# Optimization experiments

Measured on AMD Instinct MI355X. Metric: run time of the kernel, lower is better.

## Reference

```python
import jax, jax.numpy as jnp
import numpy as np

N_NODES = 50000
NEG_SLOPE = 0.2


def _gat_conv(x, edge_index, W, att_src, att_dst, bias, heads, out_ch, concat):
    """PyG-style GATConv (add_self_loops=True, negative_slope=0.2).
    x: [N, F_in], edge_index: [2, E] (row=src, row=dst), W: [F_in, heads*out_ch],
    att_src/att_dst: [heads, out_ch], bias: [heads*out_ch] or [out_ch]."""
    N = x.shape[0]
    # add self-loops
    loops = jnp.arange(N, dtype=edge_index.dtype)
    src = jnp.concatenate([edge_index[0], loops])
    dst = jnp.concatenate([edge_index[1], loops])

    h = (x @ W).reshape(N, heads, out_ch)                 # [N, H, C]
    a_src = jnp.einsum('nhc,hc->nh', h, att_src)          # [N, H]
    a_dst = jnp.einsum('nhc,hc->nh', h, att_dst)          # [N, H]

    e = a_src[src] + a_dst[dst]                           # [E', H]
    e = jnp.where(e >= 0, e, NEG_SLOPE * e)               # leaky_relu

    # segment softmax over incoming edges of each dst node
    e_max = jax.ops.segment_max(e, dst, num_segments=N)   # [N, H]
    e_max = jnp.where(jnp.isfinite(e_max), e_max, 0.0)
    ex = jnp.exp(e - e_max[dst])                          # [E', H]
    denom = jax.ops.segment_sum(ex, dst, num_segments=N)  # [N, H]
    alpha = ex / (denom[dst] + 1e-16)                     # [E', H]

    msg = alpha[:, :, None] * h[src]                      # [E', H, C]
    out = jax.ops.segment_sum(msg, dst, num_segments=N)   # [N, H, C]

    if concat:
        out = out.reshape(N, heads * out_ch)
    else:
        out = out.mean(axis=1)
    return out + bias


def setup_inputs() -> dict:
    key = jax.random.key(0)
    ks = jax.random.split(key, 12)
    F_in, hid, H1, C, H2 = 512, 8, 8, 40, 1
    x = jax.random.normal(ks[0], (N_NODES, F_in), dtype=jnp.float32)
    edge_index = jax.random.randint(ks[1], (2, 1600000), 0, N_NODES, dtype=jnp.int64)
    s1 = 1.0 / np.sqrt(F_in)
    s2 = 1.0 / np.sqrt(hid * H1)
    return {
        'x': x,
        'edge_index': edge_index,
        'W1': jax.random.normal(ks[2], (F_in, H1 * hid), dtype=jnp.float32) * s1,
        'att_src1': jax.random.normal(ks[3], (H1, hid), dtype=jnp.float32) * s2,
        'att_dst1': jax.random.normal(ks[4], (H1, hid), dtype=jnp.float32) * s2,
        'b1': jnp.zeros((H1 * hid,), dtype=jnp.float32),
        'W2': jax.random.normal(ks[5], (H1 * hid, H2 * C), dtype=jnp.float32) * s2,
        'att_src2': jax.random.normal(ks[6], (H2, C), dtype=jnp.float32) * 0.15,
        'att_dst2': jax.random.normal(ks[7], (H2, C), dtype=jnp.float32) * 0.15,
        'b2': jnp.zeros((C,), dtype=jnp.float32),
    }


def reference(x, edge_index, W1, att_src1, att_dst1, b1, W2, att_src2, att_dst2, b2):
    # eval mode: dropout is identity
    h = _gat_conv(x, edge_index, W1, att_src1, att_dst1, b1, heads=8, out_ch=8, concat=True)
    h = jax.nn.relu(h)
    h = _gat_conv(h, edge_index, W2, att_src2, att_dst2, b2, heads=1, out_ch=40, concat=False)
    return jax.nn.log_softmax(h, axis=1)
```

## Files before the change

### kernel.cpp

```cpp
#include <hip/hip_runtime.h>
#include <math.h>

#define NNODES 50000
#define NEG_SLOPE 0.2f
#define NB 391
#define BW 128
#define CHUNK 4096
#define CAP 8128

typedef __bf16 bf16x8 __attribute__((ext_vector_type(8)));
typedef float f32x4 __attribute__((ext_vector_type(4)));

__global__ void init_bcur(int* bcur) {
    int i = blockIdx.x * 256 + threadIdx.x;
    if (i < NB) bcur[i] = i * CAP;
    if (i == NB) bcur[NB] = 0;
}

__global__ __launch_bounds__(256) void bin_scatter(const int* __restrict__ ei,
                                                   int E, int N, int* bcur,
                                                   int* __restrict__ tmp) {
    __shared__ int lcnt[NB];
    __shared__ int lbase[NB];
    int tid = threadIdx.x;
    int base0 = blockIdx.x * CHUNK;
    int lim = min(base0 + CHUNK, E + N);
    for (int i = tid; i < NB; i += 256) lcnt[i] = 0;
    __syncthreads();
    for (int e = base0 + tid; e < lim; e += 256) {
        int d = (e < E) ? ei[E + e] : e - E;
        atomicAdd(&lcnt[d >> 7], 1);
    }
    __syncthreads();
    for (int b = tid; b < NB; b += 256) {
        int c = lcnt[b];
        lbase[b] = c ? atomicAdd(&bcur[b], c) : 0;
    }
    __syncthreads();
    for (int i = tid; i < NB; i += 256) lcnt[i] = 0;
    __syncthreads();
    for (int e = base0 + tid; e < lim; e += 256) {
        int s, d;
        if (e < E) { s = ei[e]; d = ei[E + e]; }
        else       { s = d = e - E; }
        int b = d >> 7;
        int p = atomicAdd(&lcnt[b], 1);
        tmp[lbase[b] + p] = ((d & 127) << 16) | s;
    }
}

__global__ __launch_bounds__(256) void csr_finalize(int* __restrict__ bcur,
                                                    const int* __restrict__ tmp,
                                                    int N, int* __restrict__ off,
                                                    int* __restrict__ off_end,
                                                    int* __restrict__ slot) {
    __shared__ int cnt[BW];
    __shared__ int cur[BW];
    __shared__ int cbase_s;
    int b = blockIdx.x, tid = threadIdx.x;
    int base = b * CAP;
    int m = bcur[b] - base;
    if (tid < BW) cnt[tid] = 0;
    __syncthreads();
    for (int i = tid; i < m; i += 256)
        atomicAdd(&cnt[(tmp[base + i] >> 16) & 127], 1);
    __syncthreads();
    if (tid == 0) cbase_s = atomicAdd(&bcur[NB], m);
    int myv = (tid < BW) ? cnt[tid] : 0;
    for (int o = 1; o < BW; o <<= 1) {
        int u = 0;
        if (tid >= o && tid < BW) u = cnt[tid - o];
        __syncthreads();
        if (tid < BW) cnt[tid] += u;
        __syncthreads();
    }
    if (tid < BW) {
        int ex = cbase_s + cnt[tid] - myv;
        cur[tid] = ex;
        int g = b * BW + tid;
        if (g < N) { off[g] = ex; off_end[g] = ex + myv; }
    }
    __syncthreads();
    for (int i = tid; i < m; i += 256) {
        int v = tmp[base + i];
        int k = (v >> 16) & 127;
        int p = atomicAdd(&cur[k], 1);
        slot[p] = v & 0xFFFF;
    }
}

__global__ void prep_w1(const float* __restrict__ W1, __bf16* __restrict__ W1b) {
    int i = blockIdx.x * 256 + threadIdx.x;
    if (i >= 512 * 64) return;
    int k = i >> 6, n = i & 63;
    W1b[((size_t)(k >> 3) * 64 + n) * 8 + (k & 7)] = (__bf16)W1[i];
}

__global__ __launch_bounds__(256) void gemm1_mfma(const float* __restrict__ X,
                                                  const __bf16* __restrict__ W1b,
                                                  const float* __restrict__ att_s1,
                                                  const float* __restrict__ att_d1,
                                                  __bf16* __restrict__ H1b,
                                                  float* __restrict__ a_s1,
                                                  float* __restrict__ a_d1,
                                                  int M) {
    __shared__ __bf16 As[2048];
    __shared__ __bf16 Bs[2048];
    int tid = threadIdx.x, wid = tid >> 6, lane = tid & 63;
    int quad = lane >> 4, l15 = lane & 15;
    int m0 = blockIdx.x * 64;
    f32x4 acc[4] = {{0.f, 0.f, 0.f, 0.f}, {0.f, 0.f, 0.f, 0.f},
                    {0.f, 0.f, 0.f, 0.f}, {0.f, 0.f, 0.f, 0.f}};
    int mrow = tid >> 2;
    int kq_w = tid & 3;
    int xrow = min(m0 + mrow, M - 1);
    const float* xp = X + (size_t)xrow * 512 + kq_w * 8;
    for (int kb = 0; kb < 16; ++kb) {
        float4 xa = *(const float4*)(xp + kb * 32);
        float4 xb = *(const float4*)(xp + kb * 32 + 4);
        bf16x8 av;
        av[0] = (__bf16)xa.x; av[1] = (__bf16)xa.y;
        av[2] = (__bf16)xa.z; av[3] = (__bf16)xa.w;
        av[4] = (__bf16)xb.x; av[5] = (__bf16)xb.y;
        av[6] = (__bf16)xb.z; av[7] = (__bf16)xb.w;
        *(bf16x8*)(As + ((size_t)kq_w * 64 + mrow) * 8) = av;
        *(bf16x8*)(Bs + ((size_t)wid * 64 + lane) * 8) =
            *(const bf16x8*)(W1b + ((size_t)(kb * 4 + wid) * 64 + lane) * 8);
        __syncthreads();
        bf16x8 af = *(const bf16x8*)(As + ((size_t)quad * 64 + 16 * wid + l15) * 8);
#pragma unroll
        for (int t = 0; t < 4; ++t) {
            bf16x8 bf = *(const bf16x8*)(Bs + ((size_t)quad * 64 + 16 * t + l15) * 8);
            acc[t] = __builtin_amdgcn_mfma_f32_16x16x32_bf16(af, bf, acc[t], 0, 0, 0);
        }
        __syncthreads();
    }
    float asv[4], adv[4];
#pragma unroll
    for (int t = 0; t < 4; ++t) {
        asv[t] = att_s1[16 * t + l15];
        adv[t] = att_d1[16 * t + l15];
    }
#pragma unroll
    for (int t = 0; t < 4; ++t) {
#pragma unroll
        for (int r = 0; r < 4; ++r) {
            int gm = m0 + 16 * wid + quad * 4 + r;
            if (gm < M) H1b[(size_t)gm * 64 + 16 * t + l15] = (__bf16)acc[t][r];
            float ps = acc[t][r] * asv[t];
            float pd = acc[t][r] * adv[t];
            ps += __shfl_xor(ps, 1); ps += __shfl_xor(ps, 2); ps += __shfl_xor(ps, 4);
            pd += __shfl_xor(pd, 1); pd += __shfl_xor(pd, 2); pd += __shfl_xor(pd, 4);
            if (gm < M && (l15 & 7) == 0) {
                int hh = 2 * t + (l15 >> 3);
                a_s1[(size_t)gm * 8 + hh] = ps;
                a_d1[(size_t)gm * 8 + hh] = pd;
            }
        }
    }
}

__global__ __launch_bounds__(256) void agg1(const int* __restrict__ off,
                                            const int* __restrict__ off_end,
                                            const int* __restrict__ slot,
                                            const __bf16* __restrict__ H1b,
                                            const float* __restrict__ a_src,
                                            const float* __restrict__ a_dst,
                                            const float* __restrict__ b1,
                                            float* __restrict__ H1R) {
    int wid = threadIdx.x >> 6, lane = threadIdx.x & 63;
    int d = blockIdx.x * 4 + wid;
    int beg = off[d], end = off_end[d];
    int h = lane >> 3;
    int eh = lane & 7;
    int es = lane >> 3;
    float adst_c = a_dst[(size_t)d * 8 + eh];
    float acc = 0.f, den_l = 0.f;
    for (int i = beg; i < end; i += 8) {
        int j = i + es;
        int jj = (j < end) ? j : (end - 1);
        int s = slot[jj];
        float e = a_src[(size_t)s * 8 + eh] + adst_c;
        e = (e >= 0.f) ? e : NEG_SLOPE * e;
        float w = (j < end) ? __expf(e) : 0.f;
        den_l += w;
#pragma unroll
        for (int q = 0; q < 8; ++q) {
            int sq = __builtin_amdgcn_readlane(s, q << 3);
            float wq = __shfl(w, (q << 3) | h);
            acc += wq * (float)H1b[(size_t)sq * 64 + lane];
        }
    }
    den_l += __shfl_xor(den_l, 8);
    den_l += __shfl_xor(den_l, 16);
    den_l += __shfl_xor(den_l, 32);
    float den = __shfl(den_l, h);
    float v = acc / (den + 1e-16f) + b1[lane];
    H1R[(size_t)d * 64 + lane] = (v > 0.f) ? v : 0.f;
}

__global__ __launch_bounds__(256) void gemm2_att2(const float* __restrict__ H1R,
                                                  const float* __restrict__ W2,
                                                  const float* __restrict__ att_src2,
                                                  const float* __restrict__ att_dst2,
                                                  __bf16* __restrict__ H2b,
                                                  float* __restrict__ a_src2,
                                                  float* __restrict__ a_dst2) {
    __shared__ float W2s[64 * 40];
    __shared__ float rows[16][64];
    int tid = threadIdx.x;
    int wid = tid >> 6, lane = tid & 63;
    for (int i = tid; i < 64 * 40; i += 256) W2s[i] = W2[i];
    int nb = blockIdx.x * 16;
#pragma unroll
    for (int r = 0; r < 4; ++r)
        rows[r * 4 + wid][lane] = H1R[(size_t)(nb + r * 4 + wid) * 64 + lane];
    __syncthreads();
    int c = lane;
    int cc = (c < 40) ? c : 0;
    float asc = att_src2[cc], adc = att_dst2[cc];
#pragma unroll
    for (int nn = 0; nn < 4; ++nn) {
        int node = nb + wid * 4 + nn;
        const float* rp = rows[wid * 4 + nn];
        float acc = 0.f;
#pragma unroll
        for (int k4 = 0; k4 < 16; ++k4) {
            float4 rv = *(const float4*)(rp + k4 * 4);
            acc += rv.x * W2s[(k4 * 4 + 0) * 40 + cc];
            acc += rv.y * W2s[(k4 * 4 + 1) * 40 + cc];
            acc += rv.z * W2s[(k4 * 4 + 2) * 40 + cc];
            acc += rv.w * W2s[(k4 * 4 + 3) * 40 + cc];
        }
        if (c < 40) H2b[(size_t)node * 40 + c] = (__bf16)acc;
        float ps = (c < 40) ? acc * asc : 0.f;
        float pd = (c < 40) ? acc * adc : 0.f;
#pragma unroll
        for (int mm = 32; mm >= 1; mm >>= 1) {
            ps += __shfl_xor(ps, mm);
            pd += __shfl_xor(pd, mm);
        }
        if (lane == 0) { a_src2[node] = ps; a_dst2[node] = pd; }
    }
}

__global__ __launch_bounds__(256) void agg2(const int* __restrict__ off,
                                            const int* __restrict__ off_end,
                                            const int* __restrict__ slot,
                                            const __bf16* __restrict__ H2b,
                                            const float* __restrict__ a_src2,
                                            const float* __restrict__ a_d2,
                                            const float* __restrict__ b2,
                                            float* __restrict__ out) {
    int wid = threadIdx.x >> 6, lane = threadIdx.x & 63;
    int d = blockIdx.x * 4 + wid;
    int beg = off[d], end = off_end[d];
    float adst = a_d2[d];
    int c = lane;
    int cc = (c < 40) ? c : 0;
    float acc = 0.f, den = 0.f;
    for (int i = beg; i < end; i += 64) {
        int j = i + lane;
        int jj = (j < end) ? j : (end - 1);
        int s = slot[jj];
        float e = a_src2[s] + adst;
        e = (e >= 0.f) ? e : NEG_SLOPE * e;
        float w = (j < end) ? __expf(e) : 0.f;
        den += w;
#pragma unroll
        for (int qb = 0; qb < 8; ++qb) {
            if (i + (qb << 3) >= end) break;
#pragma unroll
            for (int qq = 0; qq < 8; ++qq) {
                int q = (qb << 3) + qq;
                int sq = __builtin_amdgcn_readlane(s, q);
                float wq = __uint_as_float(
                    __builtin_amdgcn_readlane((int)__float_as_uint(w), q));
                acc += wq * (float)H2b[(size_t)sq * 40 + cc];
            }
        }
    }
#pragma unroll
    for (int m = 32; m >= 1; m >>= 1) den += __shfl_xor(den, m);
    float v = acc / (den + 1e-16f) + b2[cc];
    float vm = (c < 40) ? v : -3.0e38f;
#pragma unroll
    for (int m = 32; m >= 1; m >>= 1) vm = fmaxf(vm, __shfl_xor(vm, m));
    float se = (c < 40) ? __expf(v - vm) : 0.f;
#pragma unroll
    for (int m = 32; m >= 1; m >>= 1) se += __shfl_xor(se, m);
    float res = v - vm - __logf(se);
    if (c < 40) out[(size_t)d * 40 + c] = res;
}

extern "C" void kernel_launch(void* const* d_in, const int* in_sizes, int n_in,
                              void* d_out, int out_size, void* d_ws, size_t ws_size,
                              hipStream_t stream) {
    const float* x   = (const float*)d_in[0];
    const int*   ei  = (const int*)d_in[1];
    const float* W1  = (const float*)d_in[2];
    const float* as1 = (const float*)d_in[3];
    const float* ad1 = (const float*)d_in[4];
    const float* b1  = (const float*)d_in[5];
    const float* W2  = (const float*)d_in[6];
    const float* as2 = (const float*)d_in[7];
    const float* ad2 = (const float*)d_in[8];
    const float* b2  = (const float*)d_in[9];
    float* out = (float*)d_out;

    const int N = NNODES;
    const int E = in_sizes[1] / 2;
    const int total = E + N;

    char* ws = (char*)d_ws;
    size_t o = 0;
    auto alloc = [&](size_t bytes) -> void* {
        void* p = ws + o;
        o = (o + bytes + 255) & ~(size_t)255;
        return p;
    };
    int* bcur    = (int*)alloc((size_t)(NB + 1) * 4);
    int* off     = (int*)alloc((size_t)N * 4);
    int* off_end = (int*)alloc((size_t)N * 4);
    int* slot    = (int*)alloc((size_t)total * 4);
    __bf16* W1b = (__bf16*)alloc((size_t)512 * 64 * 2);
    __bf16* H1b = (__bf16*)alloc((size_t)N * 64 * 2);
    float* a_s1 = (float*)alloc((size_t)N * 8 * 4);
    float* a_d1 = (float*)alloc((size_t)N * 8 * 4);
    float* H1R  = (float*)alloc((size_t)N * 64 * 4);
    __bf16* H2b = (__bf16*)alloc((size_t)N * 40 * 2);
    float* a_s2 = (float*)alloc((size_t)N * 4);
    float* a_d2 = (float*)alloc((size_t)N * 4);
    int* tmp = (int*)H1R;
    (void)ws_size; (void)n_in; (void)out_size;

    init_bcur<<<(NB + 256) / 256, 256, 0, stream>>>(bcur);
    bin_scatter<<<(total + CHUNK - 1) / CHUNK, 256, 0, stream>>>(ei, E, N, bcur, tmp);
    csr_finalize<<<NB, 256, 0, stream>>>(bcur, tmp, N, off, off_end, slot);

    prep_w1<<<(512 * 64 + 255) / 256, 256, 0, stream>>>(W1, W1b);
    gemm1_mfma<<<(N + 63) / 64, 256, 0, stream>>>(x, W1b, as1, ad1, H1b, a_s1, a_d1, N);
    agg1<<<N / 4, 256, 0, stream>>>(off, off_end, slot, H1b, a_s1, a_d1, b1, H1R);

    gemm2_att2<<<N / 16, 256, 0, stream>>>(H1R, W2, as2, ad2, H2b, a_s2, a_d2);
    agg2<<<N / 4, 256, 0, stream>>>(off, off_end, slot, H2b, a_s2, a_d2, b2, out);
}
```

Measured before the change: 359.5 us.

## Fuse layer-2 linear transform into layer-1 aggregation and merge prep kernels

Moves the 64x40 W2 projection and the attention-score dot products into the layer-1 aggregation kernel, so the fp32 H1R intermediate is never written to or read back from global memory. The bcur init and W1 bf16 repacking are also merged into one launch, cutting two kernel launches in total. In exchange, each agg1 block now loads all of W2 into shared memory (10 KB per 4 nodes) and does a serial 64-step dot product per lane, which adds shared-memory traffic and may lower occupancy. The tmp scratch buffer gets its own workspace allocation because it no longer aliases H1R.

```diff
diff --git a/kernel.cpp b/kernel.cpp
--- a/kernel.cpp
+++ b/kernel.cpp
@@ -11,10 +11,14 @@
 typedef __bf16 bf16x8 __attribute__((ext_vector_type(8)));
 typedef float f32x4 __attribute__((ext_vector_type(4)));
 
-__global__ void init_bcur(int* bcur) {
+__global__ void prep(const float* __restrict__ W1, __bf16* __restrict__ W1b,
+                     int* __restrict__ bcur) {
     int i = blockIdx.x * 256 + threadIdx.x;
     if (i < NB) bcur[i] = i * CAP;
-    if (i == NB) bcur[NB] = 0;
+    else if (i == NB) bcur[NB] = 0;
+    if (i >= 512 * 64) return;
+    int k = i >> 6, n = i & 63;
+    W1b[((size_t)(k >> 3) * 64 + n) * 8 + (k & 7)] = (__bf16)W1[i];
 }
 
 __global__ __launch_bounds__(256) void bin_scatter(const int* __restrict__ ei,
@@ -87,13 +91,6 @@
         int p = atomicAdd(&cur[k], 1);
         slot[p] = v & 0xFFFF;
     }
-}
-
-__global__ void prep_w1(const float* __restrict__ W1, __bf16* __restrict__ W1b) {
-    int i = blockIdx.x * 256 + threadIdx.x;
-    if (i >= 512 * 64) return;
-    int k = i >> 6, n = i & 63;
-    W1b[((size_t)(k >> 3) * 64 + n) * 8 + (k & 7)] = (__bf16)W1[i];
 }
 
 __global__ __launch_bounds__(256) void gemm1_mfma(const float* __restrict__ X,
@@ -160,15 +157,25 @@
     }
 }
 
-__global__ __launch_bounds__(256) void agg1(const int* __restrict__ off,
-                                            const int* __restrict__ off_end,
-                                            const int* __restrict__ slot,
-                                            const __bf16* __restrict__ H1b,
-                                            const float* __restrict__ a_src,
-                                            const float* __restrict__ a_dst,
-                                            const float* __restrict__ b1,
-                                            float* __restrict__ H1R) {
-    int wid = threadIdx.x >> 6, lane = threadIdx.x & 63;
+__global__ __launch_bounds__(256) void agg1_fused(const int* __restrict__ off,
+                                                  const int* __restrict__ off_end,
+                                                  const int* __restrict__ slot,
+                                                  const __bf16* __restrict__ H1b,
+                                                  const float* __restrict__ a_src,
+                                                  const float* __restrict__ a_dst,
+                                                  const float* __restrict__ b1,
+                                                  const float* __restrict__ W2,
+                                                  const float* __restrict__ att_src2,
+                                                  const float* __restrict__ att_dst2,
+                                                  __bf16* __restrict__ H2b,
+                                                  float* __restrict__ a_s2,
+                                                  float* __restrict__ a_d2) {
+    __shared__ float W2s[64 * 40];
+    __shared__ float rows[4][64];
+    int tid = threadIdx.x;
+    int wid = tid >> 6, lane = tid & 63;
+    for (int i = tid; i < 64 * 40; i += 256) W2s[i] = W2[i];
+    __syncthreads();
     int d = blockIdx.x * 4 + wid;
     int beg = off[d], end = off_end[d];
     int h = lane >> 3;
@@ -196,52 +203,22 @@
     den_l += __shfl_xor(den_l, 32);
     float den = __shfl(den_l, h);
     float v = acc / (den + 1e-16f) + b1[lane];
-    H1R[(size_t)d * 64 + lane] = (v > 0.f) ? v : 0.f;
-}
-
-__global__ __launch_bounds__(256) void gemm2_att2(const float* __restrict__ H1R,
-                                                  const float* __restrict__ W2,
-                                                  const float* __restrict__ att_src2,
-                                                  const float* __restrict__ att_dst2,
-                                                  __bf16* __restrict__ H2b,
-                                                  float* __restrict__ a_src2,
-                                                  float* __restrict__ a_dst2) {
-    __shared__ float W2s[64 * 40];
-    __shared__ float rows[16][64];
-    int tid = threadIdx.x;
-    int wid = tid >> 6, lane = tid & 63;
-    for (int i = tid; i < 64 * 40; i += 256) W2s[i] = W2[i];
-    int nb = blockIdx.x * 16;
-#pragma unroll
-    for (int r = 0; r < 4; ++r)
-        rows[r * 4 + wid][lane] = H1R[(size_t)(nb + r * 4 + wid) * 64 + lane];
-    __syncthreads();
-    int c = lane;
-    int cc = (c < 40) ? c : 0;
-    float asc = att_src2[cc], adc = att_dst2[cc];
-#pragma unroll
-    for (int nn = 0; nn < 4; ++nn) {
-        int node = nb + wid * 4 + nn;
-        const float* rp = rows[wid * 4 + nn];
-        float acc = 0.f;
-#pragma unroll
-        for (int k4 = 0; k4 < 16; ++k4) {
-            float4 rv = *(const float4*)(rp + k4 * 4);
-            acc += rv.x * W2s[(k4 * 4 + 0) * 40 + cc];
-            acc += rv.y * W2s[(k4 * 4 + 1) * 40 + cc];
-            acc += rv.z * W2s[(k4 * 4 + 2) * 40 + cc];
-            acc += rv.w * W2s[(k4 * 4 + 3) * 40 + cc];
-        }
-        if (c < 40) H2b[(size_t)node * 40 + c] = (__bf16)acc;
-        float ps = (c < 40) ? acc * asc : 0.f;
-        float pd = (c < 40) ? acc * adc : 0.f;
-#pragma unroll
-        for (int mm = 32; mm >= 1; mm >>= 1) {
-            ps += __shfl_xor(ps, mm);
-            pd += __shfl_xor(pd, mm);
-        }
-        if (lane == 0) { a_src2[node] = ps; a_dst2[node] = pd; }
-    }
+    v = (v > 0.f) ? v : 0.f;
+    rows[wid][lane] = v;
+    int c = lane, cc = (c < 40) ? c : 0;
+    float acc2 = 0.f;
+    const float* rp = rows[wid];
+#pragma unroll 8
+    for (int k = 0; k < 64; ++k) acc2 += rp[k] * W2s[k * 40 + cc];
+    if (c < 40) H2b[(size_t)d * 40 + c] = (__bf16)acc2;
+    float ps = (c < 40) ? acc2 * att_src2[cc] : 0.f;
+    float pd = (c < 40) ? acc2 * att_dst2[cc] : 0.f;
+#pragma unroll
+    for (int mm = 32; mm >= 1; mm >>= 1) {
+        ps += __shfl_xor(ps, mm);
+        pd += __shfl_xor(pd, mm);
+    }
+    if (lane == 0) { a_s2[d] = ps; a_d2[d] = pd; }
 }
 
 __global__ __launch_bounds__(256) void agg2(const int* __restrict__ off,
@@ -323,25 +300,24 @@
     int* off     = (int*)alloc((size_t)N * 4);
     int* off_end = (int*)alloc((size_t)N * 4);
     int* slot    = (int*)alloc((size_t)total * 4);
+    int* tmp     = (int*)alloc((size_t)NB * CAP * 4);
     __bf16* W1b = (__bf16*)alloc((size_t)512 * 64 * 2);
     __bf16* H1b = (__bf16*)alloc((size_t)N * 64 * 2);
     float* a_s1 = (float*)alloc((size_t)N * 8 * 4);
     float* a_d1 = (float*)alloc((size_t)N * 8 * 4);
-    float* H1R  = (float*)alloc((size_t)N * 64 * 4);
     __bf16* H2b = (__bf16*)alloc((size_t)N * 40 * 2);
     float* a_s2 = (float*)alloc((size_t)N * 4);
     float* a_d2 = (float*)alloc((size_t)N * 4);
-    int* tmp = (int*)H1R;
     (void)ws_size; (void)n_in; (void)out_size;
 
-    init_bcur<<<(NB + 256) / 256, 256, 0, stream>>>(bcur);
+    prep<<<(512 * 64 + 255) / 256, 256, 0, stream>>>(W1, W1b, bcur);
     bin_scatter<<<(total + CHUNK - 1) / CHUNK, 256, 0, stream>>>(ei, E, N, bcur, tmp);
     csr_finalize<<<NB, 256, 0, stream>>>(bcur, tmp, N, off, off_end, slot);
 
-    prep_w1<<<(512 * 64 + 255) / 256, 256, 0, stream>>>(W1, W1b);
     gemm1_mfma<<<(N + 63) / 64, 256, 0, stream>>>(x, W1b, as1, ad1, H1b, a_s1, a_d1, N);
-    agg1<<<N / 4, 256, 0, stream>>>(off, off_end, slot, H1b, a_s1, a_d1, b1, H1R);
-
-    gemm2_att2<<<N / 16, 256, 0, stream>>>(H1R, W2, as2, ad2, H2b, a_s2, a_d2);
+
+    agg1_fused<<<N / 4, 256, 0, stream>>>(off, off_end, slot, H1b, a_s1, a_d1, b1,
+                                          W2, as2, ad2, H2b, a_s2, a_d2);
+
     agg2<<<N / 4, 256, 0, stream>>>(off, off_end, slot, H2b, a_s2, a_d2, b2, out);
 }
```

New measurement: 353.1 us. Within noise of the previous version (-1.8%).
